# Optimization experiments

Measured on AMD Instinct MI355X. Metric: run time of the kernel, lower is better.

## Reference

```python
import jax, jax.numpy as jnp
import numpy as np


def setup_inputs() -> dict:
    key = jax.random.key(0)
    k1, k2, k3 = jax.random.split(key, 3)
    Lq, Lkv, H, D = 2048, 2048, 16, 128
    return {
        "query": jax.random.normal(k1, (Lq, H, D), dtype=jnp.float32),
        "key": jax.random.normal(k2, (Lkv, H, D), dtype=jnp.float32),
        "value": jax.random.normal(k3, (Lkv, H, D), dtype=jnp.float32),
    }


def reference(query, key, value):
    # query: [Lq, H, D], key: [Lkv, H, D], value: [Lkv, H, Dv]
    # Original module performs chunked online-softmax attention; the math is
    # exactly scaled-dot-product softmax attention with scale 1/sqrt(k_features).
    d = query.shape[-1]
    q = query * (1.0 / jnp.sqrt(jnp.asarray(d, dtype=query.dtype)))
    scores = jnp.einsum('qhd,khd->qhk', q, key)          # [Lq, H, Lkv]
    weights = jax.nn.softmax(scores, axis=-1)            # numerically stable online softmax equivalent
    out = jnp.einsum('qhk,khf->qhf', weights, value)     # [Lq, H, Dv]
    return out
```

## Files before the change

kernel.cpp:

```cpp
#include <hip/hip_runtime.h>
#include <hip/hip_bf16.h>

typedef __bf16 bf16x8 __attribute__((ext_vector_type(8)));
typedef __bf16 bf16x4 __attribute__((ext_vector_type(4)));
typedef float  f32x16 __attribute__((ext_vector_type(16)));
typedef float  f32x4  __attribute__((ext_vector_type(4)));

#define HD     2048
#define DH     128
#define KVT    64
#define NCH    16
#define NSPLIT 2
#define NROWS  32768
#define TILE_ELEMS 8192

__device__ __forceinline__ void glds16(const void* g, void* l) {
    typedef const __attribute__((address_space(1))) void g_as_t;
    typedef __attribute__((address_space(3))) void l_as_t;
    __builtin_amdgcn_global_load_lds((g_as_t*)g, (l_as_t*)l, 16, 0, 0);
}

__global__ __launch_bounds__(256, 8)
void prep_k(const float* __restrict__ Kg, __bf16* __restrict__ wsK)
{
    const int kv = blockIdx.x;
    const int t  = threadIdx.x;
    const int h  = t >> 4, c8 = t & 15;
    const float* src = Kg + (size_t)kv * HD + h * DH + c8 * 8;
    f32x4 a = *(const f32x4*)(src);
    f32x4 b = *(const f32x4*)(src + 4);
    bf16x8 o;
    o[0]=(__bf16)a[0]; o[1]=(__bf16)a[1]; o[2]=(__bf16)a[2]; o[3]=(__bf16)a[3];
    o[4]=(__bf16)b[0]; o[5]=(__bf16)b[1]; o[6]=(__bf16)b[2]; o[7]=(__bf16)b[3];
    __bf16* dst = wsK + ((size_t)(h * 32 + (kv >> 6)) * TILE_ELEMS)
                      + (kv & 63) * 128 + ((c8 ^ (kv & 15)) << 3);
    *(bf16x8*)dst = o;
}

__global__ __launch_bounds__(256, 4)
void prep_vt(const float* __restrict__ Vg, __bf16* __restrict__ wsV)
{
    __shared__ float tile[32][33];
    const int b = blockIdx.x;
    const int dvb = b & 3, kvb = (b >> 2) & 63, h = b >> 8;
    const int t = threadIdx.x;
    {
        const int kvl = t >> 3, dv4 = (t & 7) * 4;
        f32x4 v = *(const f32x4*)(Vg + (size_t)(kvb * 32 + kvl) * HD + h * DH + dvb * 32 + dv4);
        tile[kvl][dv4 + 0] = v[0]; tile[kvl][dv4 + 1] = v[1];
        tile[kvl][dv4 + 2] = v[2]; tile[kvl][dv4 + 3] = v[3];
    }
    __syncthreads();
    {
        const int dvl = t >> 3, kv4 = (t & 7) * 4;
        const int dv   = dvb * 32 + dvl;
        const int T    = kvb >> 1;
        const int kloc = (kvb & 1) * 32 + kv4;
        const int kg   = kloc >> 3;
        bf16x4 o;
        o[0] = (__bf16)tile[kv4 + 0][dvl]; o[1] = (__bf16)tile[kv4 + 1][dvl];
        o[2] = (__bf16)tile[kv4 + 2][dvl]; o[3] = (__bf16)tile[kv4 + 3][dvl];
        __bf16* dst = wsV + ((size_t)(h * 32 + T) * TILE_ELEMS)
                          + dv * 64 + (((kg ^ (dv & 7)) << 3) + (kloc & 7));
        *(bf16x4*)dst = o;
    }
}

__global__ __launch_bounds__(256, 2)
void fmha_main(const float* __restrict__ Qg,
               const __bf16* __restrict__ wsK, const __bf16* __restrict__ wsV,
               float* __restrict__ wsO, float* __restrict__ wsML)
{
    __shared__ __align__(16) __bf16 klds[2][TILE_ELEMS];
    __shared__ __align__(16) __bf16 vlds[2][TILE_ELEMS];

    const int tid  = threadIdx.x;
    const int lane = tid & 63;
    const int wrp  = tid >> 6;
    const int g    = lane >> 5;
    const int l31  = lane & 31;

    const int b    = blockIdx.x;
    const int grp  = b & 31;
    const int qblk = b >> 5;
    const int h    = grp >> 1;
    const int sp   = grp & 1;
    const int T0   = sp * NCH;

    const float qscale = 1.4426950408889634f * 0.08838834764831845f;
    const int q = qblk * 128 + wrp * 32 + l31;

    bf16x8 qf[8];
    {
        const float* qrow = Qg + (size_t)q * HD + h * DH;
        #pragma unroll
        for (int j = 0; j < 8; ++j) {
            f32x4 a = *(const f32x4*)(qrow + j * 16 + 8 * g);
            f32x4 c = *(const f32x4*)(qrow + j * 16 + 8 * g + 4);
            bf16x8 f;
            f[0] = (__bf16)(a[0] * qscale); f[1] = (__bf16)(a[1] * qscale);
            f[2] = (__bf16)(a[2] * qscale); f[3] = (__bf16)(a[3] * qscale);
            f[4] = (__bf16)(c[0] * qscale); f[5] = (__bf16)(c[1] * qscale);
            f[6] = (__bf16)(c[2] * qscale); f[7] = (__bf16)(c[3] * qscale);
            qf[j] = f;
        }
    }

    auto stage = [&](int T, int buf) {
        const char* kt = (const char*)(wsK + (size_t)(h * 32 + T) * TILE_ELEMS) + lane * 16;
        const char* vt = (const char*)(wsV + (size_t)(h * 32 + T) * TILE_ELEMS) + lane * 16;
        char* kl = (char*)&klds[buf][0];
        char* vl = (char*)&vlds[buf][0];
        #pragma unroll
        for (int i = 0; i < 4; ++i) {
            const int c = (i * 4 + wrp) * 1024;
            glds16(kt + c, kl + c);
            glds16(vt + c, vl + c);
        }
    };

    auto sync_all = []() {
        asm volatile("s_waitcnt vmcnt(0) lgkmcnt(0)" ::: "memory");
        __builtin_amdgcn_s_barrier();
    };

    float mrun = -1e30f, lrun = 0.0f;
    f32x16 o0, o1, o2, o3;
    #pragma unroll
    for (int r = 0; r < 16; ++r) { o0[r] = 0.f; o1[r] = 0.f; o2[r] = 0.f; o3[r] = 0.f; }

    stage(T0, 0);
    sync_all();

    const int ksw  = l31 & 15;
    const int vkey = l31 & 7;

    #pragma unroll 2
    for (int tt = 0; tt < NCH; ++tt) {
        const int cur = tt & 1;
        if (tt + 1 < NCH) stage(T0 + tt + 1, cur ^ 1);

        f32x16 s0, s1;
        #pragma unroll
        for (int r = 0; r < 16; ++r) { s0[r] = 0.f; s1[r] = 0.f; }
        __builtin_amdgcn_s_setprio(1);
        #pragma unroll
        for (int j = 0; j < 8; ++j) {
            const int gcol = ((2 * j + g) ^ ksw) << 3;
            bf16x8 k0 = *(const bf16x8*)&klds[cur][l31 * 128 + gcol];
            s0 = __builtin_amdgcn_mfma_f32_32x32x16_bf16(k0, qf[j], s0, 0, 0, 0);
            bf16x8 k1 = *(const bf16x8*)&klds[cur][(32 + l31) * 128 + gcol];
            s1 = __builtin_amdgcn_mfma_f32_32x32x16_bf16(k1, qf[j], s1, 0, 0, 0);
        }
        __builtin_amdgcn_s_setprio(0);

        float m16[8];
        #pragma unroll
        for (int r = 0; r < 8; ++r)
            m16[r] = fmaxf(fmaxf(s0[r], s0[r + 8]), fmaxf(s1[r], s1[r + 8]));
        float tmax = fmaxf(fmaxf(fmaxf(m16[0], m16[4]), fmaxf(m16[1], m16[5])),
                           fmaxf(fmaxf(m16[2], m16[6]), fmaxf(m16[3], m16[7])));
        tmax = fmaxf(tmax, __shfl_xor(tmax, 32, 64));

        if (__any(tmax > mrun + 8.0f)) {
            const float mnew  = fmaxf(mrun, tmax);
            const float alpha = __builtin_amdgcn_exp2f(mrun - mnew);
            lrun *= alpha;
            #pragma unroll
            for (int r = 0; r < 16; ++r) { o0[r]*=alpha; o1[r]*=alpha; o2[r]*=alpha; o3[r]*=alpha; }
            mrun = mnew;
        }

        #pragma unroll
        for (int r = 0; r < 16; ++r) {
            s0[r] = __builtin_amdgcn_exp2f(s0[r] - mrun);
            s1[r] = __builtin_amdgcn_exp2f(s1[r] - mrun);
        }
        float ps = 0.f;
        #pragma unroll
        for (int r = 0; r < 16; ++r) ps += s0[r] + s1[r];
        lrun += ps;

        bf16x8 pf0, pf1, pf2, pf3;
        #pragma unroll
        for (int e = 0; e < 8; ++e) {
            pf0[e] = (__bf16)s0[e]; pf1[e] = (__bf16)s0[8 + e];
            pf2[e] = (__bf16)s1[e]; pf3[e] = (__bf16)s1[8 + e];
        }

        __builtin_amdgcn_s_setprio(1);
        #pragma unroll
        for (int bb = 0; bb < 4; ++bb) {
            const __bf16* vb = &vlds[cur][(bb * 32 + l31) * 64];
            f32x16& oo = (bb == 0) ? o0 : (bb == 1) ? o1 : (bb == 2) ? o2 : o3;
            #define PVSTEP(mm, pf)                                                \
            {                                                                     \
                bf16x4 a0 = *(const bf16x4*)(vb + (((2*(mm))   ^ vkey) << 3) + 4*g);\
                bf16x4 a1 = *(const bf16x4*)(vb + (((2*(mm)+1) ^ vkey) << 3) + 4*g);\
                bf16x8 va;                                                        \
                va[0]=a0[0]; va[1]=a0[1]; va[2]=a0[2]; va[3]=a0[3];               \
                va[4]=a1[0]; va[5]=a1[1]; va[6]=a1[2]; va[7]=a1[3];               \
                oo = __builtin_amdgcn_mfma_f32_32x32x16_bf16(va, pf, oo, 0, 0, 0);\
            }
            PVSTEP(0, pf0) PVSTEP(1, pf1) PVSTEP(2, pf2) PVSTEP(3, pf3)
            #undef PVSTEP
        }
        __builtin_amdgcn_s_setprio(0);

        if (tt + 1 < NCH) sync_all();
    }

    const float ltot  = lrun + __shfl_xor(lrun, 32, 64);
    const int   rowid = q * 16 + h;

    float* orow = wsO + ((size_t)sp * NROWS + rowid) * 128;
    #pragma unroll
    for (int bb = 0; bb < 4; ++bb) {
        const f32x16& oo = (bb == 0) ? o0 : (bb == 1) ? o1 : (bb == 2) ? o2 : o3;
        #pragma unroll
        for (int jj = 0; jj < 4; ++jj) {
            f32x4 v;
            v[0] = oo[4*jj+0]; v[1] = oo[4*jj+1]; v[2] = oo[4*jj+2]; v[3] = oo[4*jj+3];
            *(f32x4*)(orow + bb * 32 + 8 * jj + 4 * g) = v;
        }
    }
    if (lane < 32) {
        float* ml = wsML + ((size_t)sp * NROWS + rowid) * 2;
        ml[0] = mrun;
        ml[1] = ltot;
    }
}

__global__ __launch_bounds__(256, 4)
void fmha_combine(const float* __restrict__ wsO, const float* __restrict__ wsML,
                  float* __restrict__ Og)
{
    const int tid   = threadIdx.x;
    const int rowid = blockIdx.x * 8 + (tid >> 5);
    const int c     = (tid & 31) * 4;

    float m[NSPLIT], l[NSPLIT];
    float M = -1e30f;
    #pragma unroll
    for (int s = 0; s < NSPLIT; ++s) {
        const float* ml = wsML + ((size_t)s * NROWS + rowid) * 2;
        m[s] = ml[0]; l[s] = ml[1];
        M = fmaxf(M, m[s]);
    }
    float L = 0.f, w[NSPLIT];
    #pragma unroll
    for (int s = 0; s < NSPLIT; ++s) {
        w[s] = __builtin_amdgcn_exp2f(m[s] - M);
        L += l[s] * w[s];
    }
    const float inv = 1.0f / L;

    f32x4 acc; acc[0]=0.f; acc[1]=0.f; acc[2]=0.f; acc[3]=0.f;
    #pragma unroll
    for (int s = 0; s < NSPLIT; ++s) {
        f32x4 v = *(const f32x4*)(wsO + ((size_t)s * NROWS + rowid) * 128 + c);
        acc[0] += v[0] * w[s]; acc[1] += v[1] * w[s];
        acc[2] += v[2] * w[s]; acc[3] += v[3] * w[s];
    }
    f32x4 r;
    r[0] = acc[0]*inv; r[1] = acc[1]*inv; r[2] = acc[2]*inv; r[3] = acc[3]*inv;
    *(f32x4*)(Og + (size_t)rowid * 128 + c) = r;
}

__global__ __launch_bounds__(256, 2)
void fmha_fb(const float* __restrict__ Qg, const float* __restrict__ Kg,
             const float* __restrict__ Vg, float* __restrict__ Og)
{
    __shared__ __align__(16) __bf16 klds[2][32 * 128];
    __shared__ __align__(16) __bf16 vtlds[2][DH * 36];

    const int tid  = threadIdx.x;
    const int lane = tid & 63;
    const int wrp  = tid >> 6;
    const int g    = lane >> 5;
    const int l31  = lane & 31;

    const int b    = blockIdx.x;
    const int h    = 2 * (b & 7) + ((b >> 3) >> 4);
    const int qblk = (b >> 3) & 15;

    const float qscale = 1.4426950408889634f * 0.08838834764831845f;
    const int q = qblk * 128 + wrp * 32 + l31;

    bf16x8 qf[8];
    {
        const float* qrow = Qg + (size_t)q * HD + h * DH;
        #pragma unroll
        for (int db = 0; db < 8; ++db) {
            f32x4 a = *(const f32x4*)(qrow + db * 16 + 8 * g);
            f32x4 c = *(const f32x4*)(qrow + db * 16 + 8 * g + 4);
            bf16x8 f;
            f[0] = (__bf16)(a[0] * qscale); f[1] = (__bf16)(a[1] * qscale);
            f[2] = (__bf16)(a[2] * qscale); f[3] = (__bf16)(a[3] * qscale);
            f[4] = (__bf16)(c[0] * qscale); f[5] = (__bf16)(c[1] * qscale);
            f[6] = (__bf16)(c[2] * qscale); f[7] = (__bf16)(c[3] * qscale);
            qf[db] = f;
        }
    }

    const int krow = tid >> 3, kc = tid & 7;
    const int vkv  = tid & 31, vdv0 = (tid >> 5) * 16;
    const float* kbase = Kg + (size_t)h * DH;
    const float* vbase = Vg + (size_t)h * DH;

    f32x4 kreg0, kreg1, kreg2, kreg3, vreg0, vreg1, vreg2, vreg3;

    auto stage_load = [&](int t) {
        const float* kp = kbase + (size_t)(t * 32 + krow) * HD + kc * 8;
        kreg0 = *(const f32x4*)(kp);
        kreg1 = *(const f32x4*)(kp + 4);
        kreg2 = *(const f32x4*)(kp + 64);
        kreg3 = *(const f32x4*)(kp + 68);
        const float* vp = vbase + (size_t)(t * 32 + vkv) * HD + vdv0;
        vreg0 = *(const f32x4*)(vp);
        vreg1 = *(const f32x4*)(vp + 4);
        vreg2 = *(const f32x4*)(vp + 8);
        vreg3 = *(const f32x4*)(vp + 12);
    };

    auto stage_write = [&](int buf) {
        bf16x8 k0, k1;
        k0[0]=(__bf16)kreg0[0]; k0[1]=(__bf16)kreg0[1]; k0[2]=(__bf16)kreg0[2]; k0[3]=(__bf16)kreg0[3];
        k0[4]=(__bf16)kreg1[0]; k0[5]=(__bf16)kreg1[1]; k0[6]=(__bf16)kreg1[2]; k0[7]=(__bf16)kreg1[3];
        k1[0]=(__bf16)kreg2[0]; k1[1]=(__bf16)kreg2[1]; k1[2]=(__bf16)kreg2[2]; k1[3]=(__bf16)kreg2[3];
        k1[4]=(__bf16)kreg3[0]; k1[5]=(__bf16)kreg3[1]; k1[6]=(__bf16)kreg3[2]; k1[7]=(__bf16)kreg3[3];
        const int swz = (krow & 7) << 3;
        *(bf16x8*)&klds[buf][krow * 128 + ((kc * 8) ^ swz)]      = k0;
        *(bf16x8*)&klds[buf][krow * 128 + ((kc * 8 + 64) ^ swz)] = k1;
        #pragma unroll
        for (int jj = 0; jj < 4; ++jj) {
            f32x4 vv = (jj == 0) ? vreg0 : (jj == 1) ? vreg1 : (jj == 2) ? vreg2 : vreg3;
            #pragma unroll
            for (int e = 0; e < 4; ++e)
                vtlds[buf][(vdv0 + jj * 4 + e) * 36 + vkv] = (__bf16)vv[e];
        }
    };

    float mrun = -1e30f, lrun = 0.0f;
    f32x16 o0, o1, o2, o3;
    #pragma unroll
    for (int r = 0; r < 16; ++r) { o0[r] = 0.f; o1[r] = 0.f; o2[r] = 0.f; o3[r] = 0.f; }

    stage_load(0);
    stage_write(0);

    for (int tt = 0; tt < 64; ++tt) {
        const int cur = tt & 1;
        if (tt + 1 < 64) stage_load(tt + 1);
        __syncthreads();

        f32x16 sa, sb;
        #pragma unroll
        for (int r = 0; r < 16; ++r) { sa[r] = 0.f; sb[r] = 0.f; }
        const int kswz = (l31 & 7) << 3;
        #pragma unroll
        for (int db = 0; db < 4; ++db) {
            bf16x8 kfa = *(const bf16x8*)&klds[cur][l31 * 128 + (((2*db)   * 16 + g * 8) ^ kswz)];
            sa = __builtin_amdgcn_mfma_f32_32x32x16_bf16(kfa, qf[2*db],   sa, 0, 0, 0);
            bf16x8 kfb = *(const bf16x8*)&klds[cur][l31 * 128 + (((2*db+1) * 16 + g * 8) ^ kswz)];
            sb = __builtin_amdgcn_mfma_f32_32x32x16_bf16(kfb, qf[2*db+1], sb, 0, 0, 0);
        }
        f32x16 s;
        #pragma unroll
        for (int r = 0; r < 16; ++r) s[r] = sa[r] + sb[r];

        float m8[8];
        #pragma unroll
        for (int r = 0; r < 8; ++r) m8[r] = fmaxf(s[r], s[r + 8]);
        float tmax = fmaxf(fmaxf(fmaxf(m8[0], m8[4]), fmaxf(m8[1], m8[5])),
                           fmaxf(fmaxf(m8[2], m8[6]), fmaxf(m8[3], m8[7])));
        tmax = fmaxf(tmax, __shfl_xor(tmax, 32, 64));

        if (__any(tmax > mrun + 8.0f)) {
            const float mnew  = fmaxf(mrun, tmax);
            const float alpha = __builtin_amdgcn_exp2f(mrun - mnew);
            lrun *= alpha;
            #pragma unroll
            for (int r = 0; r < 16; ++r) { o0[r] *= alpha; o1[r] *= alpha; o2[r] *= alpha; o3[r] *= alpha; }
            mrun = mnew;
        }

        float p[16];
        #pragma unroll
        for (int r = 0; r < 16; ++r) p[r] = __builtin_amdgcn_exp2f(s[r] - mrun);
        float ps0 = 0, ps1 = 0, ps2 = 0, ps3 = 0;
        #pragma unroll
        for (int r = 0; r < 4; ++r) { ps0 += p[r]; ps1 += p[r+4]; ps2 += p[r+8]; ps3 += p[r+12]; }
        lrun += ((ps0 + ps1) + (ps2 + ps3));

        bf16x8 pf0, pf1;
        #pragma unroll
        for (int e = 0; e < 8; ++e) { pf0[e] = (__bf16)p[e]; pf1[e] = (__bf16)p[8 + e]; }

        #pragma unroll
        for (int bb = 0; bb < 4; ++bb) {
            const __bf16* vb = &vtlds[cur][(bb * 32 + l31) * 36];
            bf16x4 a0 = *(const bf16x4*)(vb + 4 * g);
            bf16x4 a1 = *(const bf16x4*)(vb + 8 + 4 * g);
            bf16x8 va;
            va[0]=a0[0]; va[1]=a0[1]; va[2]=a0[2]; va[3]=a0[3];
            va[4]=a1[0]; va[5]=a1[1]; va[6]=a1[2]; va[7]=a1[3];
            f32x16& oo = (bb == 0) ? o0 : (bb == 1) ? o1 : (bb == 2) ? o2 : o3;
            oo = __builtin_amdgcn_mfma_f32_32x32x16_bf16(va, pf0, oo, 0, 0, 0);
            bf16x4 b0 = *(const bf16x4*)(vb + 16 + 4 * g);
            bf16x4 b1 = *(const bf16x4*)(vb + 24 + 4 * g);
            va[0]=b0[0]; va[1]=b0[1]; va[2]=b0[2]; va[3]=b0[3];
            va[4]=b1[0]; va[5]=b1[1]; va[6]=b1[2]; va[7]=b1[3];
            oo = __builtin_amdgcn_mfma_f32_32x32x16_bf16(va, pf1, oo, 0, 0, 0);
        }

        if (tt + 1 < 64) stage_write(cur ^ 1);
    }

    const float ltot = lrun + __shfl_xor(lrun, 32, 64);
    const float inv  = 1.0f / ltot;
    float* orow = Og + ((size_t)q * 16 + h) * 128;
    #pragma unroll
    for (int bb = 0; bb < 4; ++bb) {
        const f32x16& oo = (bb == 0) ? o0 : (bb == 1) ? o1 : (bb == 2) ? o2 : o3;
        #pragma unroll
        for (int jj = 0; jj < 4; ++jj) {
            f32x4 v;
            v[0] = oo[4*jj+0] * inv; v[1] = oo[4*jj+1] * inv;
            v[2] = oo[4*jj+2] * inv; v[3] = oo[4*jj+3] * inv;
            *(f32x4*)(orow + bb * 32 + 8 * jj + 4 * g) = v;
        }
    }
}

extern "C" void kernel_launch(void* const* d_in, const int* in_sizes, int n_in,
                              void* d_out, int out_size, void* d_ws, size_t ws_size,
                              hipStream_t stream) {
    const float* Q = (const float*)d_in[0];
    const float* K = (const float*)d_in[1];
    const float* V = (const float*)d_in[2];
    float* O = (float*)d_out;

    const size_t kv_bytes = (size_t)512 * TILE_ELEMS * 2;
    const size_t needO  = (size_t)NSPLIT * NROWS * 128;
    const size_t needML = (size_t)NSPLIT * NROWS * 2;
    const size_t need_bytes = 2 * kv_bytes + (needO + needML) * sizeof(float);

    if (ws_size >= need_bytes) {
        __bf16* wsK = (__bf16*)d_ws;
        __bf16* wsV = (__bf16*)((char*)d_ws + kv_bytes);
        float*  wsO = (float*)((char*)d_ws + 2 * kv_bytes);
        float*  wsML = wsO + needO;
        hipLaunchKernelGGL(prep_k,  dim3(2048), dim3(256), 0, stream, K, wsK);
        hipLaunchKernelGGL(prep_vt, dim3(4096), dim3(256), 0, stream, V, wsV);
        hipLaunchKernelGGL(fmha_main, dim3(512), dim3(256), 0, stream,
                           Q, wsK, wsV, wsO, wsML);
        hipLaunchKernelGGL(fmha_combine, dim3(NROWS / 8), dim3(256), 0, stream,
                           wsO, wsML, O);
    } else {
        hipLaunchKernelGGL(fmha_fb, dim3(256), dim3(256), 0, stream, Q, K, V, O);
    }
}
```

Measured before the change: 74.78 us.

## Merge prep kernels, fuse split-KV combine via atomic counter, repad V layout

Merges the K and V preparation kernels into one launch, and replaces the separate combine kernel with an in-kernel last-arriver merge: each split block writes its partial output, increments a per-pair atomic counter, and the second arriver reads the other partial and writes the final normalized output. The V tile layout changes from an XOR swizzle to a padded row stride of 68, and the K swizzle key changes to reduce LDS bank conflicts. This removes two launches and most of the combine's global traffic, but adds a memset, threadfences, and a serialized tail for the late block.

```diff
diff --git a/kernel.cpp b/kernel.cpp
--- a/kernel.cpp
+++ b/kernel.cpp
@@ -6,13 +6,14 @@
 typedef float  f32x16 __attribute__((ext_vector_type(16)));
 typedef float  f32x4  __attribute__((ext_vector_type(4)));
 
-#define HD     2048
-#define DH     128
-#define KVT    64
-#define NCH    16
-#define NSPLIT 2
-#define NROWS  32768
-#define TILE_ELEMS 8192
+#define HD      2048
+#define DH      128
+#define KVT     64
+#define NCH     16
+#define NSPLIT  2
+#define NROWS   32768
+#define KTILE_E 8192
+#define VTILE_E 8704
 
 __device__ __forceinline__ void glds16(const void* g, void* l) {
     typedef const __attribute__((address_space(1))) void g_as_t;
@@ -20,59 +21,64 @@
     __builtin_amdgcn_global_load_lds((g_as_t*)g, (l_as_t*)l, 16, 0, 0);
 }
 
-__global__ __launch_bounds__(256, 8)
-void prep_k(const float* __restrict__ Kg, __bf16* __restrict__ wsK)
-{
-    const int kv = blockIdx.x;
-    const int t  = threadIdx.x;
-    const int h  = t >> 4, c8 = t & 15;
-    const float* src = Kg + (size_t)kv * HD + h * DH + c8 * 8;
-    f32x4 a = *(const f32x4*)(src);
-    f32x4 b = *(const f32x4*)(src + 4);
-    bf16x8 o;
-    o[0]=(__bf16)a[0]; o[1]=(__bf16)a[1]; o[2]=(__bf16)a[2]; o[3]=(__bf16)a[3];
-    o[4]=(__bf16)b[0]; o[5]=(__bf16)b[1]; o[6]=(__bf16)b[2]; o[7]=(__bf16)b[3];
-    __bf16* dst = wsK + ((size_t)(h * 32 + (kv >> 6)) * TILE_ELEMS)
-                      + (kv & 63) * 128 + ((c8 ^ (kv & 15)) << 3);
-    *(bf16x8*)dst = o;
+__device__ __forceinline__ int kkey_of(int r) {
+    return (r & 7) ^ (((r >> 3) & 3) << 1);
 }
 
 __global__ __launch_bounds__(256, 4)
-void prep_vt(const float* __restrict__ Vg, __bf16* __restrict__ wsV)
+void prep_kv(const float* __restrict__ Kg, const float* __restrict__ Vg,
+             __bf16* __restrict__ wsK, __bf16* __restrict__ wsV)
 {
     __shared__ float tile[32][33];
-    const int b = blockIdx.x;
-    const int dvb = b & 3, kvb = (b >> 2) & 63, h = b >> 8;
-    const int t = threadIdx.x;
-    {
-        const int kvl = t >> 3, dv4 = (t & 7) * 4;
-        f32x4 v = *(const f32x4*)(Vg + (size_t)(kvb * 32 + kvl) * HD + h * DH + dvb * 32 + dv4);
-        tile[kvl][dv4 + 0] = v[0]; tile[kvl][dv4 + 1] = v[1];
-        tile[kvl][dv4 + 2] = v[2]; tile[kvl][dv4 + 3] = v[3];
-    }
-    __syncthreads();
-    {
-        const int dvl = t >> 3, kv4 = (t & 7) * 4;
-        const int dv   = dvb * 32 + dvl;
-        const int T    = kvb >> 1;
-        const int kloc = (kvb & 1) * 32 + kv4;
-        const int kg   = kloc >> 3;
-        bf16x4 o;
-        o[0] = (__bf16)tile[kv4 + 0][dvl]; o[1] = (__bf16)tile[kv4 + 1][dvl];
-        o[2] = (__bf16)tile[kv4 + 2][dvl]; o[3] = (__bf16)tile[kv4 + 3][dvl];
-        __bf16* dst = wsV + ((size_t)(h * 32 + T) * TILE_ELEMS)
-                          + dv * 64 + (((kg ^ (dv & 7)) << 3) + (kloc & 7));
-        *(bf16x4*)dst = o;
+    const int bid = blockIdx.x;
+    if (bid < 2048) {
+        const int kv = bid;
+        const int t  = threadIdx.x;
+        const int h  = t >> 4, c8 = t & 15;
+        const float* src = Kg + (size_t)kv * HD + h * DH + c8 * 8;
+        f32x4 a = *(const f32x4*)(src);
+        f32x4 b = *(const f32x4*)(src + 4);
+        bf16x8 o;
+        o[0]=(__bf16)a[0]; o[1]=(__bf16)a[1]; o[2]=(__bf16)a[2]; o[3]=(__bf16)a[3];
+        o[4]=(__bf16)b[0]; o[5]=(__bf16)b[1]; o[6]=(__bf16)b[2]; o[7]=(__bf16)b[3];
+        const int r = kv & 63;
+        __bf16* dst = wsK + ((size_t)(h * 32 + (kv >> 6)) * KTILE_E)
+                          + r * 128 + ((c8 ^ kkey_of(r)) << 3);
+        *(bf16x8*)dst = o;
+    } else {
+        const int b = bid - 2048;
+        const int dvb = b & 3, kvb = (b >> 2) & 63, h = b >> 8;
+        const int t = threadIdx.x;
+        {
+            const int kvl = t >> 3, dv4 = (t & 7) * 4;
+            f32x4 v = *(const f32x4*)(Vg + (size_t)(kvb * 32 + kvl) * HD + h * DH + dvb * 32 + dv4);
+            tile[kvl][dv4 + 0] = v[0]; tile[kvl][dv4 + 1] = v[1];
+            tile[kvl][dv4 + 2] = v[2]; tile[kvl][dv4 + 3] = v[3];
+        }
+        __syncthreads();
+        {
+            const int dvl = t >> 3, kv4 = (t & 7) * 4;
+            const int dv   = dvb * 32 + dvl;
+            const int T    = kvb >> 1;
+            const int kloc = (kvb & 1) * 32 + kv4;
+            bf16x4 o;
+            o[0] = (__bf16)tile[kv4 + 0][dvl]; o[1] = (__bf16)tile[kv4 + 1][dvl];
+            o[2] = (__bf16)tile[kv4 + 2][dvl]; o[3] = (__bf16)tile[kv4 + 3][dvl];
+            __bf16* dst = wsV + ((size_t)(h * 32 + T) * VTILE_E) + dv * 68 + kloc;
+            *(bf16x4*)dst = o;
+        }
     }
 }
 
 __global__ __launch_bounds__(256, 2)
 void fmha_main(const float* __restrict__ Qg,
                const __bf16* __restrict__ wsK, const __bf16* __restrict__ wsV,
-               float* __restrict__ wsO, float* __restrict__ wsML)
+               float* __restrict__ wsO, float* __restrict__ wsML,
+               int* __restrict__ cnt, float* __restrict__ Og)
 {
-    __shared__ __align__(16) __bf16 klds[2][TILE_ELEMS];
-    __shared__ __align__(16) __bf16 vlds[2][TILE_ELEMS];
+    __shared__ __align__(16) __bf16 klds[2][KTILE_E];
+    __shared__ __align__(16) __bf16 vlds[2][VTILE_E];
+    __shared__ int role;
 
     const int tid  = threadIdx.x;
     const int lane = tid & 63;
@@ -107,16 +113,15 @@
     }
 
     auto stage = [&](int T, int buf) {
-        const char* kt = (const char*)(wsK + (size_t)(h * 32 + T) * TILE_ELEMS) + lane * 16;
-        const char* vt = (const char*)(wsV + (size_t)(h * 32 + T) * TILE_ELEMS) + lane * 16;
-        char* kl = (char*)&klds[buf][0];
-        char* vl = (char*)&vlds[buf][0];
-        #pragma unroll
-        for (int i = 0; i < 4; ++i) {
-            const int c = (i * 4 + wrp) * 1024;
-            glds16(kt + c, kl + c);
-            glds16(vt + c, vl + c);
-        }
+        const char* kt = (const char*)(wsK + (size_t)(h * 32 + T) * KTILE_E) + wrp * 1024 + lane * 16;
+        char* kl = (char*)&klds[buf][0] + wrp * 1024;
+        #pragma unroll
+        for (int i = 0; i < 4; ++i) glds16(kt + i * 4096, kl + i * 4096);
+        const char* vt = (const char*)(wsV + (size_t)(h * 32 + T) * VTILE_E) + wrp * 1024 + lane * 16;
+        char* vl = (char*)&vlds[buf][0] + wrp * 1024;
+        #pragma unroll
+        for (int i = 0; i < 4; ++i) glds16(vt + i * 4096, vl + i * 4096);
+        if (wrp == 0) glds16(vt + 16384, vl + 16384);
     };
 
     auto sync_all = []() {
@@ -132,8 +137,7 @@
     stage(T0, 0);
     sync_all();
 
-    const int ksw  = l31 & 15;
-    const int vkey = l31 & 7;
+    const int kkey = kkey_of(l31);
 
     #pragma unroll 2
     for (int tt = 0; tt < NCH; ++tt) {
@@ -146,7 +150,7 @@
         __builtin_amdgcn_s_setprio(1);
         #pragma unroll
         for (int j = 0; j < 8; ++j) {
-            const int gcol = ((2 * j + g) ^ ksw) << 3;
+            const int gcol = ((2 * j + g) ^ kkey) << 3;
             bf16x8 k0 = *(const bf16x8*)&klds[cur][l31 * 128 + gcol];
             s0 = __builtin_amdgcn_mfma_f32_32x32x16_bf16(k0, qf[j], s0, 0, 0, 0);
             bf16x8 k1 = *(const bf16x8*)&klds[cur][(32 + l31) * 128 + gcol];
@@ -191,18 +195,18 @@
         __builtin_amdgcn_s_setprio(1);
         #pragma unroll
         for (int bb = 0; bb < 4; ++bb) {
-            const __bf16* vb = &vlds[cur][(bb * 32 + l31) * 64];
+            const __bf16* vb = &vlds[cur][(bb * 32 + l31) * 68];
             f32x16& oo = (bb == 0) ? o0 : (bb == 1) ? o1 : (bb == 2) ? o2 : o3;
-            #define PVSTEP(mm, pf)                                                \
+            #define PVSTEP(base, pf)                                              \
             {                                                                     \
-                bf16x4 a0 = *(const bf16x4*)(vb + (((2*(mm))   ^ vkey) << 3) + 4*g);\
-                bf16x4 a1 = *(const bf16x4*)(vb + (((2*(mm)+1) ^ vkey) << 3) + 4*g);\
+                bf16x4 a0 = *(const bf16x4*)(vb + (base) + 4 * g);                \
+                bf16x4 a1 = *(const bf16x4*)(vb + (base) + 8 + 4 * g);            \
                 bf16x8 va;                                                        \
                 va[0]=a0[0]; va[1]=a0[1]; va[2]=a0[2]; va[3]=a0[3];               \
                 va[4]=a1[0]; va[5]=a1[1]; va[6]=a1[2]; va[7]=a1[3];               \
                 oo = __builtin_amdgcn_mfma_f32_32x32x16_bf16(va, pf, oo, 0, 0, 0);\
             }
-            PVSTEP(0, pf0) PVSTEP(1, pf1) PVSTEP(2, pf2) PVSTEP(3, pf3)
+            PVSTEP(0,  pf0) PVSTEP(16, pf1) PVSTEP(32, pf2) PVSTEP(48, pf3)
             #undef PVSTEP
         }
         __builtin_amdgcn_s_setprio(0);
@@ -212,8 +216,9 @@
 
     const float ltot  = lrun + __shfl_xor(lrun, 32, 64);
     const int   rowid = q * 16 + h;
-
-    float* orow = wsO + ((size_t)sp * NROWS + rowid) * 128;
+    const int   pair  = qblk * 16 + h;
+
+    float* myO = wsO + ((size_t)sp * NROWS + rowid) * 128;
     #pragma unroll
     for (int bb = 0; bb < 4; ++bb) {
         const f32x16& oo = (bb == 0) ? o0 : (bb == 1) ? o1 : (bb == 2) ? o2 : o3;
@@ -221,7 +226,7 @@
         for (int jj = 0; jj < 4; ++jj) {
             f32x4 v;
             v[0] = oo[4*jj+0]; v[1] = oo[4*jj+1]; v[2] = oo[4*jj+2]; v[3] = oo[4*jj+3];
-            *(f32x4*)(orow + bb * 32 + 8 * jj + 4 * g) = v;
+            *(f32x4*)(myO + bb * 32 + 8 * jj + 4 * g) = v;
         }
     }
     if (lane < 32) {
@@ -229,42 +234,43 @@
         ml[0] = mrun;
         ml[1] = ltot;
     }
-}
-
-__global__ __launch_bounds__(256, 4)
-void fmha_combine(const float* __restrict__ wsO, const float* __restrict__ wsML,
-                  float* __restrict__ Og)
-{
-    const int tid   = threadIdx.x;
-    const int rowid = blockIdx.x * 8 + (tid >> 5);
-    const int c     = (tid & 31) * 4;
-
-    float m[NSPLIT], l[NSPLIT];
-    float M = -1e30f;
-    #pragma unroll
-    for (int s = 0; s < NSPLIT; ++s) {
-        const float* ml = wsML + ((size_t)s * NROWS + rowid) * 2;
-        m[s] = ml[0]; l[s] = ml[1];
-        M = fmaxf(M, m[s]);
-    }
-    float L = 0.f, w[NSPLIT];
-    #pragma unroll
-    for (int s = 0; s < NSPLIT; ++s) {
-        w[s] = __builtin_amdgcn_exp2f(m[s] - M);
-        L += l[s] * w[s];
-    }
-    const float inv = 1.0f / L;
-
-    f32x4 acc; acc[0]=0.f; acc[1]=0.f; acc[2]=0.f; acc[3]=0.f;
-    #pragma unroll
-    for (int s = 0; s < NSPLIT; ++s) {
-        f32x4 v = *(const f32x4*)(wsO + ((size_t)s * NROWS + rowid) * 128 + c);
-        acc[0] += v[0] * w[s]; acc[1] += v[1] * w[s];
-        acc[2] += v[2] * w[s]; acc[3] += v[3] * w[s];
-    }
-    f32x4 r;
-    r[0] = acc[0]*inv; r[1] = acc[1]*inv; r[2] = acc[2]*inv; r[3] = acc[3]*inv;
-    *(f32x4*)(Og + (size_t)rowid * 128 + c) = r;
+    __threadfence();
+    __syncthreads();
+    if (tid == 0) role = atomicAdd(&cnt[pair], 1);
+    __syncthreads();
+
+    if (role == 1) {
+        __threadfence();
+        const int osp = sp ^ 1;
+        const float* oml = wsML + ((size_t)osp * NROWS + rowid) * 2;
+        const float mo = oml[0], lo = oml[1];
+        const float m0 = (sp == 0) ? mrun : mo;
+        const float l0 = (sp == 0) ? ltot : lo;
+        const float m1 = (sp == 0) ? mo : mrun;
+        const float l1 = (sp == 0) ? lo : ltot;
+        const float M  = fmaxf(m0, m1);
+        const float w0 = __builtin_amdgcn_exp2f(m0 - M);
+        const float w1 = __builtin_amdgcn_exp2f(m1 - M);
+        const float inv = 1.0f / (l0 * w0 + l1 * w1);
+        const float wm = (sp == 0) ? w0 : w1;
+        const float wo = (sp == 0) ? w1 : w0;
+        const float* oO = wsO + ((size_t)osp * NROWS + rowid) * 128;
+        float* orow = Og + (size_t)rowid * 128;
+        #pragma unroll
+        for (int bb = 0; bb < 4; ++bb) {
+            const f32x16& oo = (bb == 0) ? o0 : (bb == 1) ? o1 : (bb == 2) ? o2 : o3;
+            #pragma unroll
+            for (int jj = 0; jj < 4; ++jj) {
+                f32x4 v = *(const f32x4*)(oO + bb * 32 + 8 * jj + 4 * g);
+                f32x4 r;
+                r[0] = (oo[4*jj+0] * wm + v[0] * wo) * inv;
+                r[1] = (oo[4*jj+1] * wm + v[1] * wo) * inv;
+                r[2] = (oo[4*jj+2] * wm + v[2] * wo) * inv;
+                r[3] = (oo[4*jj+3] * wm + v[3] * wo) * inv;
+                *(f32x4*)(orow + bb * 32 + 8 * jj + 4 * g) = r;
+            }
+        }
+    }
 }
 
 __global__ __launch_bounds__(256, 2)
@@ -441,22 +447,23 @@
     const float* V = (const float*)d_in[2];
     float* O = (float*)d_out;
 
-    const size_t kv_bytes = (size_t)512 * TILE_ELEMS * 2;
+    const size_t wsK_b = (size_t)512 * KTILE_E * 2;
+    const size_t wsV_b = (size_t)512 * VTILE_E * 2;
     const size_t needO  = (size_t)NSPLIT * NROWS * 128;
     const size_t needML = (size_t)NSPLIT * NROWS * 2;
-    const size_t need_bytes = 2 * kv_bytes + (needO + needML) * sizeof(float);
+    const size_t cnt_b  = 256 * sizeof(int);
+    const size_t need_bytes = wsK_b + wsV_b + (needO + needML) * sizeof(float) + cnt_b;
 
     if (ws_size >= need_bytes) {
         __bf16* wsK = (__bf16*)d_ws;
-        __bf16* wsV = (__bf16*)((char*)d_ws + kv_bytes);
-        float*  wsO = (float*)((char*)d_ws + 2 * kv_bytes);
+        __bf16* wsV = (__bf16*)((char*)d_ws + wsK_b);
+        float*  wsO = (float*)((char*)d_ws + wsK_b + wsV_b);
         float*  wsML = wsO + needO;
-        hipLaunchKernelGGL(prep_k,  dim3(2048), dim3(256), 0, stream, K, wsK);
-        hipLaunchKernelGGL(prep_vt, dim3(4096), dim3(256), 0, stream, V, wsV);
+        int*    cnt  = (int*)(wsML + needML);
+        hipMemsetAsync(cnt, 0, cnt_b, stream);
+        hipLaunchKernelGGL(prep_kv, dim3(6144), dim3(256), 0, stream, K, V, wsK, wsV);
         hipLaunchKernelGGL(fmha_main, dim3(512), dim3(256), 0, stream,
-                           Q, wsK, wsV, wsO, wsML);
-        hipLaunchKernelGGL(fmha_combine, dim3(NROWS / 8), dim3(256), 0, stream,
-                           wsO, wsML, O);
+                           Q, wsK, wsV, wsO, wsML, cnt, O);
     } else {
         hipLaunchKernelGGL(fmha_fb, dim3(256), dim3(256), 0, stream, Q, K, V, O);
     }
```

After: 207.9 us. 2.78x slower.
